# Kernel tuning notes

Measured on AMD Instinct MI355X. Metric: run time of the kernel, lower is better.

The kernel has to match this reference:

```python
import jax, jax.numpy as jnp
import numpy as np

BSIZE = 20
KEEP = 0.5  # 1 - dropout_rate


def setup_inputs() -> dict:
    key = jax.random.key(0)
    ks = jax.random.split(key, 8)
    B, N, C = 1, 262144, 128
    H = 300
    x = jax.random.normal(ks[0], (B, N, 2 * C), dtype=jnp.float32)
    ind = jax.random.randint(ks[1], (131072,), 0, B * N, dtype=jnp.int64)
    W1 = jax.random.normal(ks[2], (H, 2 * C), dtype=jnp.float32) * 0.05
    b1 = jnp.zeros((H,), dtype=jnp.float32)
    W2 = jax.random.normal(ks[3], (H, H), dtype=jnp.float32) * 0.05
    b2 = jnp.zeros((H,), dtype=jnp.float32)
    W3 = jax.random.normal(ks[4], (1, H), dtype=jnp.float32) * 0.05
    b3 = jnp.zeros((1,), dtype=jnp.float32)
    return {"x": x, "ind": ind, "W1": W1, "b1": b1, "W2": W2, "b2": b2, "W3": W3, "b3": b3}


def reference(x, ind, W1, b1, W2, b2, W3, b3):
    B, N, D = x.shape
    C = D // 2
    xf = x.reshape(B * N, D)
    xi = xf[ind]                     # [n, 2C] gathered joint samples
    n = ind.shape[0]

    def mlp(h, dkey):
        h = jax.nn.relu(h @ W1.T + b1)          # fc1 + relu
        h = h @ W2.T + b2                        # fc2
        mask = jax.random.bernoulli(dkey, KEEP, h.shape)
        h = jnp.where(mask, h / KEEP, jnp.float32(0))  # dropout
        h = jax.nn.relu(h)
        return h @ W3.T + b3                     # fc3 -> [n, 1]

    def step(acc, key):
        kp, k1, k2 = jax.random.split(key, 3)
        perm = jax.random.permutation(kp, n)
        z1 = mlp(xi, k1)
        # marginal: first-half features from ind, second-half from permuted ind
        xm = jnp.concatenate([xi[:, :C], xi[perm, C:]], axis=1)
        z2 = mlp(xm, k2)
        # mean(z1) - log(mean(exp(z2))) computed stably
        mi = jnp.mean(z1) - (jax.nn.logsumexp(z2) - jnp.log(jnp.float32(n)))
        return acc + mi, None

    keys = jax.random.split(jax.random.key(42), BSIZE)
    total, _ = jax.lax.scan(step, jnp.float32(0.0), keys)
    return total / BSIZE
```

## Files before the change

kernel.cpp:

```cpp
#include <hip/hip_runtime.h>
#include <hip/hip_fp16.h>


#define N_SAMP  131072
#define NMASK   (N_SAMP - 1)
#define HH      300
#define HPAD    320
#define DD      256
#define KPASS   20
#define PSTRIDE 320

#define OFF_S    ((size_t)0)
#define OFF_B1P  ((size_t)1024)
#define OFF_B2P  ((size_t)2304)
#define OFF_W3P  ((size_t)3584)
#define OFF_C2   ((size_t)4864)
#define OFF_W1B  ((size_t)8192)
#define OFF_W2B  (OFF_W1B + (size_t)163840)
#define OFF_P    (OFF_W2B + (size_t)204800)
#define OFF_Q    (OFF_P + (size_t)N_SAMP*PSTRIDE*2)

typedef _Float16 f16x8 __attribute__((ext_vector_type(8)));
typedef float    fx4   __attribute__((ext_vector_type(4)));

__global__ void prep_kernel(const float* __restrict__ W1, const float* __restrict__ b1,
                            const float* __restrict__ W2, const float* __restrict__ b2,
                            const float* __restrict__ W3, char* __restrict__ ws)
{
    double* S     = (double*)(ws + OFF_S);
    float* b1p    = (float*)(ws + OFF_B1P);
    float* b2p    = (float*)(ws + OFF_B2P);
    float* w3p    = (float*)(ws + OFF_W3P);
    float* c2p    = (float*)(ws + OFF_C2);
    _Float16* w1b = (_Float16*)(ws + OFF_W1B);
    _Float16* w2b = (_Float16*)(ws + OFF_W2B);
    int tid = blockIdx.x * blockDim.x + threadIdx.x;
    int nth = gridDim.x * blockDim.x;
    if (tid <= KPASS) S[tid] = 0.0;
    for (int i = tid; i < HPAD; i += nth) {
        b1p[i] = (i < HH) ? b1[i] : 0.f;
        b2p[i] = (i < HH) ? b2[i] : 0.f;
        w3p[i] = (i < HH) ? W3[i] : 0.f;
        c2p[i] = (i < HH) ? 2.8853900817779268f * W3[i] : 0.f;
    }
    for (int i = tid; i < 20 * 8 * 64 * 8; i += nth) {
        const int j = i & 7, lane = (i >> 3) & 63, rem = i >> 9;
        const int kt = rem & 7, nt = rem >> 3;
        const int n = nt * 16 + (lane & 15);
        const int k = kt * 32 + (lane >> 4) * 8 + j;
        w1b[i] = (n < HH) ? (_Float16)W1[n * DD + k] : (_Float16)0.f;
    }
    for (int i = tid; i < 4 * 50 * 64 * 8; i += nth) {
        const int j = i & 7, lane = (i >> 3) & 63, rem = i >> 9;
        const int nq = rem / 50, r2 = rem - nq * 50;
        const int kt = r2 / 5,  nn = r2 - kt * 5;
        const int nt = nq * 5 + nn;
        const int n = nt * 16 + (lane & 15);
        const int k = kt * 32 + (lane >> 4) * 8 + j;
        float v = 0.f;
        if (n < HH) {
            if (k < HH)       v = W2[n * HH + k];
            else if (k == HH) v = b2[n];
        }
        w2b[i] = (_Float16)v;
    }
}

__global__ __launch_bounds__(256, 2)
void fc1_kernel(const float* __restrict__ x, const int* __restrict__ ind,
                char* __restrict__ ws)
{
    const _Float16* w1b = (const _Float16*)(ws + OFF_W1B);
    const float* b1p    = (const float*)(ws + OFF_B1P);
    const int i0 = blockIdx.x * 128;

    __shared__ __align__(16) char lds[65536];
    _Float16* At  = (_Float16*)lds;
    _Float16* buf = (_Float16*)lds;

    const int t    = threadIdx.x;
    const int lane = t & 63, w = t >> 6;
    const int tx   = lane & 15, quad = lane >> 4;
    const int colw = w * 80;

    {
        const int m = t >> 1, c = t & 1;
        const int mt = m >> 4, ml = m & 15;
        const int r = ind[i0 + m];
        const float* xr = x + (size_t)r * DD;
        #pragma unroll
        for (int i = 0; i < 16; ++i) {
            const int ch = 2 * i + c;
            const int kt = ch >> 2, qd = ch & 3;
            const float4 f0 = *(const float4*)(xr + ch * 8);
            const float4 f1 = *(const float4*)(xr + ch * 8 + 4);
            f16x8 h;
            h[0] = (_Float16)f0.x; h[1] = (_Float16)f0.y;
            h[2] = (_Float16)f0.z; h[3] = (_Float16)f0.w;
            h[4] = (_Float16)f1.x; h[5] = (_Float16)f1.y;
            h[6] = (_Float16)f1.z; h[7] = (_Float16)f1.w;
            *(f16x8*)(At + ((size_t)(kt * 8 + mt) * 64 + ml * 4 + qd) * 8) = h;
        }
    }
    __syncthreads();

    #pragma unroll
    for (int ph = 0; ph < 2; ++ph) {
        fx4 acc[8][5] = {};
        #pragma unroll
        for (int kt = 0; kt < 4; ++kt) {
            const int ktg = ph * 4 + kt;
            f16x8 bf[5];
            #pragma unroll
            for (int n = 0; n < 5; ++n)
                bf[n] = *(const f16x8*)(w1b + ((size_t)((w * 5 + n) * 8 + ktg) * 64 + lane) * 8);
            #pragma unroll
            for (int mh = 0; mh < 2; ++mh) {
                f16x8 af[4];
                #pragma unroll
                for (int mi = 0; mi < 4; ++mi)
                    af[mi] = *(const f16x8*)(At + ((size_t)(ktg * 8 + mh * 4 + mi) * 64 + tx * 4 + quad) * 8);
                #pragma unroll
                for (int mi = 0; mi < 4; ++mi)
                    #pragma unroll
                    for (int n = 0; n < 5; ++n)
                        acc[mh * 4 + mi][n] =
                            __builtin_amdgcn_mfma_f32_16x16x32_f16(af[mi], bf[n], acc[mh * 4 + mi][n], 0, 0, 0);
            }
        }
        _Float16* out = (_Float16*)(ws + (ph ? OFF_Q : OFF_P));
        #pragma unroll
        for (int g = 0; g < 4; ++g) {
            __syncthreads();
            #pragma unroll
            for (int mi = 0; mi < 2; ++mi) {
                const int mt = g * 2 + mi;
                #pragma unroll
                for (int n = 0; n < 5; ++n) {
                    const int col = colw + n * 16 + tx;
                    const float bb = (ph == 0) ? b1p[col] : 0.f;
                    #pragma unroll
                    for (int r = 0; r < 4; ++r) {
                        const int row32 = mi * 16 + quad * 4 + r;
                        buf[row32 * 328 + col] = (_Float16)(acc[mt][n][r] + bb);
                    }
                }
            }
            __syncthreads();
            #pragma unroll
            for (int s5 = 0; s5 < 5; ++s5) {
                const int idx = t + s5 * 256;
                const int rr = idx / 40, cc = idx - rr * 40;
                *(uint4*)(out + (size_t)(i0 + g * 32 + rr) * PSTRIDE + cc * 8) =
                    *(const uint4*)(buf + rr * 328 + cc * 8);
            }
        }
        __syncthreads();
    }
}

__global__ __launch_bounds__(256, 3)
void fc23_kernel(char* __restrict__ ws)
{
    const _Float16* w2b = (const _Float16*)(ws + OFF_W2B);
    const float* w3p = (const float*)(ws + OFF_W3P);
    const float* c2p = (const float*)(ws + OFF_C2);
    const _Float16* P = (const _Float16*)(ws + OFF_P);
    const _Float16* Q = (const _Float16*)(ws + OFF_Q);
    double* S = (double*)(ws + OFF_S);

    const int p  = blockIdx.y;
    const int i0 = blockIdx.x * 64;
    const unsigned shift = (p == 0) ? 0u : (((unsigned)p * 2654435761u) & NMASK);

    __shared__ __align__(16) char lds[40960 + 1024];
    _Float16* At = (_Float16*)lds;
    float* part = (float*)(lds + 40960);

    const int t    = threadIdx.x;
    const int lane = t & 63, w = t >> 6;
    const int tx   = lane & 15, quad = lane >> 4;
    const int colw = w * 80;

    const _Float16* wb = w2b + (size_t)(w * 50) * 512 + (size_t)lane * 8;
    f16x8 bA[5], bB[5];
    #pragma unroll
    for (int n = 0; n < 5; ++n) bA[n] = *(const f16x8*)(wb + (size_t)n * 512);

    {
        const int c = t & 3, m = t >> 2;
        const int mt = m >> 4, ml = m & 15;
        const int prow = i0 + m;
        int ws_ = ml * 4 + c;  ws_ ^= (ws_ >> 3) & 3;
        const _Float16* pr = P + (size_t)prow * PSTRIDE;
        const _Float16* qr = Q + (size_t)(((unsigned)prow + shift) & NMASK) * PSTRIDE;
        #pragma unroll
        for (int i = 0; i < 10; ++i) {
            const int ch = c + 4 * i;
            f16x8 hp = *(const f16x8*)(pr + ch * 8);
            f16x8 hq = *(const f16x8*)(qr + ch * 8);
            f16x8 sv = hp + hq;
            sv = __builtin_elementwise_max(sv, (f16x8)(_Float16)0);
            if (i == 9 && c == 1) sv[4] = (_Float16)1.f;
            *(f16x8*)(At + ((size_t)(mt * 10 + i) * 64 + ws_) * 8) = sv;
        }
    }
    __syncthreads();

    int rs = tx * 4 + quad;  rs ^= (rs >> 3) & 3;

    fx4 acc[4][5] = {};
    #pragma unroll
    for (int kt = 0; kt < 10; ++kt) {
        f16x8* bc = (kt & 1) ? bB : bA;
        f16x8* bn = (kt & 1) ? bA : bB;
        if (kt < 9) {
            #pragma unroll
            for (int n = 0; n < 5; ++n)
                bn[n] = *(const f16x8*)(wb + (size_t)((kt + 1) * 5 + n) * 512);
        }
        f16x8 af[4];
        #pragma unroll
        for (int mi = 0; mi < 4; ++mi)
            af[mi] = *(const f16x8*)(At + ((size_t)(mi * 10 + kt) * 64 + rs) * 8);
        #pragma unroll
        for (int mi = 0; mi < 4; ++mi)
            #pragma unroll
            for (int n = 0; n < 5; ++n)
                acc[mi][n] =
                    __builtin_amdgcn_mfma_f32_16x16x32_f16(af[mi], bc[n], acc[mi][n], 0, 0, 0);
    }

    float w3v[5], c2v[5];
    #pragma unroll
    for (int n = 0; n < 5; ++n) {
        w3v[n] = w3p[colw + n * 16 + tx];
        c2v[n] = c2p[colw + n * 16 + tx];
    }
    #pragma unroll
    for (int mi = 0; mi < 4; ++mi) {
        float ps[4];
        if (p == 0) {
            ps[0] = ps[1] = ps[2] = ps[3] = 0.f;
            #pragma unroll
            for (int n = 0; n < 5; ++n)
                #pragma unroll
                for (int r = 0; r < 4; ++r)
                    ps[r] = fmaf(w3v[n], fmaxf(acc[mi][n][r], 0.f), ps[r]);
        } else {
            float prd[4] = {1.f, 1.f, 1.f, 1.f};
            #pragma unroll
            for (int n = 0; n < 5; ++n)
                #pragma unroll
                for (int r = 0; r < 4; ++r) {
                    const float hr = fmaxf(acc[mi][n][r], 0.f);
                    const float u  = __builtin_amdgcn_exp2f(c2v[n] * hr);
                    prd[r] *= fmaf(0.5f, u, 0.5f);
                }
            #pragma unroll
            for (int r = 0; r < 4; ++r)
                ps[r] = __builtin_amdgcn_logf(prd[r]);
        }
        #pragma unroll
        for (int r = 0; r < 4; ++r) {
            float v = ps[r];
            v += __shfl_xor(v, 1); v += __shfl_xor(v, 2);
            v += __shfl_xor(v, 4); v += __shfl_xor(v, 8);
            ps[r] = v;
        }
        if (tx == 0) {
            #pragma unroll
            for (int r = 0; r < 4; ++r)
                part[(mi * 16 + quad * 4 + r) * 4 + w] = ps[r];
        }
    }
    __syncthreads();

    if (t < 64) {
        const float4 pv = *(const float4*)(part + t * 4);
        const float s = pv.x + pv.y + pv.z + pv.w;
        float tot = (p == 0) ? s : __builtin_amdgcn_exp2f(s);
        tot += __shfl_xor(tot, 1);  tot += __shfl_xor(tot, 2);
        tot += __shfl_xor(tot, 4);  tot += __shfl_xor(tot, 8);
        tot += __shfl_xor(tot, 16); tot += __shfl_xor(tot, 32);
        if (t == 0) atomicAdd(&S[p], (double)tot);
    }
}

__global__ void fin_kernel(char* __restrict__ ws, float* __restrict__ out)
{
    if (threadIdx.x == 0 && blockIdx.x == 0) {
        const double* S = (const double*)(ws + OFF_S);
        double m1 = S[0] / (double)N_SAMP;
        double a = 0.0;
        for (int p = 1; p <= KPASS; ++p) a += log(S[p] / (double)N_SAMP);
        out[0] = (float)(m1 - a / (double)KPASS);
    }
}

extern "C" void kernel_launch(void* const* d_in, const int* in_sizes, int n_in,
                              void* d_out, int out_size, void* d_ws, size_t ws_size,
                              hipStream_t stream)
{
    const float* x  = (const float*)d_in[0];
    const int* ind  = (const int*)d_in[1];
    const float* W1 = (const float*)d_in[2];
    const float* b1 = (const float*)d_in[3];
    const float* W2 = (const float*)d_in[4];
    const float* b2 = (const float*)d_in[5];
    const float* W3 = (const float*)d_in[6];
    char* ws = (char*)d_ws;

    hipLaunchKernelGGL(prep_kernel, dim3(512), dim3(256), 0, stream, W1, b1, W2, b2, W3, ws);
    hipLaunchKernelGGL(fc1_kernel, dim3(N_SAMP / 128), dim3(256), 0, stream, x, ind, ws);
    hipLaunchKernelGGL(fc23_kernel, dim3(N_SAMP / 64, KPASS + 1), dim3(256), 0, stream, ws);
    hipLaunchKernelGGL(fin_kernel, dim3(1), dim3(64), 0, stream, ws, (float*)d_out);
}
```

Baseline: 1.118 ms.

## Stage P/Q tiles into LDS via direct global-to-LDS loads, combine in MFMA loop

The fc23 kernel now copies raw P and Q rows straight into LDS with global_load_lds instead of loading them through registers, adding, applying ReLU and storing. The add and ReLU move into the MFMA k-loop, done on LDS reads of both tiles. The bias-1 column is produced by adding 0.5 in each of the P and Q producers instead of being patched in. LDS use doubles to 80KB and occupancy drops from 3 to 2 blocks per CU, with extra LDS reads and vector ops inside the inner loop.

```diff
diff --git a/kernel.cpp b/kernel.cpp
--- a/kernel.cpp
+++ b/kernel.cpp
@@ -22,6 +22,13 @@
 
 typedef _Float16 f16x8 __attribute__((ext_vector_type(8)));
 typedef float    fx4   __attribute__((ext_vector_type(4)));
+
+__device__ __forceinline__ void gload_lds16(const void* g, void* l)
+{
+    __builtin_amdgcn_global_load_lds(
+        (const __attribute__((address_space(1))) void*)g,
+        (__attribute__((address_space(3))) void*)l, 16, 0, 0);
+}
 
 __global__ void prep_kernel(const float* __restrict__ W1, const float* __restrict__ b1,
                             const float* __restrict__ W2, const float* __restrict__ b2,
@@ -38,7 +45,7 @@
     int nth = gridDim.x * blockDim.x;
     if (tid <= KPASS) S[tid] = 0.0;
     for (int i = tid; i < HPAD; i += nth) {
-        b1p[i] = (i < HH) ? b1[i] : 0.f;
+        b1p[i] = (i < HH) ? b1[i] : ((i == HH) ? 0.5f : 0.f);
         b2p[i] = (i < HH) ? b2[i] : 0.f;
         w3p[i] = (i < HH) ? W3[i] : 0.f;
         c2p[i] = (i < HH) ? 2.8853900817779268f * W3[i] : 0.f;
@@ -138,7 +145,8 @@
                 #pragma unroll
                 for (int n = 0; n < 5; ++n) {
                     const int col = colw + n * 16 + tx;
-                    const float bb = (ph == 0) ? b1p[col] : 0.f;
+                    const float bb = (ph == 0) ? b1p[col]
+                                               : ((col == HH) ? 0.5f : 0.f);
                     #pragma unroll
                     for (int r = 0; r < 4; ++r) {
                         const int row32 = mi * 16 + quad * 4 + r;
@@ -159,7 +167,7 @@
     }
 }
 
-__global__ __launch_bounds__(256, 3)
+__global__ __launch_bounds__(256, 2)
 void fc23_kernel(char* __restrict__ ws)
 {
     const _Float16* w2b = (const _Float16*)(ws + OFF_W2B);
@@ -173,38 +181,37 @@
     const int i0 = blockIdx.x * 64;
     const unsigned shift = (p == 0) ? 0u : (((unsigned)p * 2654435761u) & NMASK);
 
-    __shared__ __align__(16) char lds[40960 + 1024];
-    _Float16* At = (_Float16*)lds;
-    float* part = (float*)(lds + 40960);
+    __shared__ __align__(16) char lds[81920];
+    _Float16* Pt = (_Float16*)lds;
+    _Float16* Qt = (_Float16*)(lds + 40960);
+    float* part  = (float*)lds;
 
     const int t    = threadIdx.x;
     const int lane = t & 63, w = t >> 6;
     const int tx   = lane & 15, quad = lane >> 4;
     const int colw = w * 80;
 
+    {
+        const int g = lane ^ ((lane >> 3) & 3);
+        const int prow = i0 + w * 16 + (g >> 2);
+        const unsigned qrow = ((unsigned)prow + shift) & NMASK;
+        const char* psrc = (const char*)(P + (size_t)prow * PSTRIDE) + (g & 3) * 16;
+        const char* qsrc = (const char*)(Q + (size_t)qrow * PSTRIDE) + (g & 3) * 16;
+        char* pdst = (char*)Pt + w * 10240;
+        char* qdst = (char*)Qt + w * 10240;
+        #pragma unroll
+        for (int kt = 0; kt < 10; ++kt) {
+            gload_lds16(psrc + kt * 64, pdst + kt * 1024);
+            gload_lds16(qsrc + kt * 64, qdst + kt * 1024);
+        }
+    }
+
     const _Float16* wb = w2b + (size_t)(w * 50) * 512 + (size_t)lane * 8;
     f16x8 bA[5], bB[5];
     #pragma unroll
     for (int n = 0; n < 5; ++n) bA[n] = *(const f16x8*)(wb + (size_t)n * 512);
 
-    {
-        const int c = t & 3, m = t >> 2;
-        const int mt = m >> 4, ml = m & 15;
-        const int prow = i0 + m;
-        int ws_ = ml * 4 + c;  ws_ ^= (ws_ >> 3) & 3;
-        const _Float16* pr = P + (size_t)prow * PSTRIDE;
-        const _Float16* qr = Q + (size_t)(((unsigned)prow + shift) & NMASK) * PSTRIDE;
-        #pragma unroll
-        for (int i = 0; i < 10; ++i) {
-            const int ch = c + 4 * i;
-            f16x8 hp = *(const f16x8*)(pr + ch * 8);
-            f16x8 hq = *(const f16x8*)(qr + ch * 8);
-            f16x8 sv = hp + hq;
-            sv = __builtin_elementwise_max(sv, (f16x8)(_Float16)0);
-            if (i == 9 && c == 1) sv[4] = (_Float16)1.f;
-            *(f16x8*)(At + ((size_t)(mt * 10 + i) * 64 + ws_) * 8) = sv;
-        }
-    }
+    asm volatile("s_waitcnt vmcnt(0)" ::: "memory");
     __syncthreads();
 
     int rs = tx * 4 + quad;  rs ^= (rs >> 3) & 3;
@@ -221,8 +228,13 @@
         }
         f16x8 af[4];
         #pragma unroll
-        for (int mi = 0; mi < 4; ++mi)
-            af[mi] = *(const f16x8*)(At + ((size_t)(mi * 10 + kt) * 64 + rs) * 8);
+        for (int mi = 0; mi < 4; ++mi) {
+            const size_t o = ((size_t)(mi * 10 + kt) * 64 + rs) * 8;
+            f16x8 ap = *(const f16x8*)(Pt + o);
+            f16x8 aq = *(const f16x8*)(Qt + o);
+            f16x8 sv = ap + aq;
+            af[mi] = __builtin_elementwise_max(sv, (f16x8)(_Float16)0);
+        }
         #pragma unroll
         for (int mi = 0; mi < 4; ++mi)
             #pragma unroll
@@ -237,6 +249,7 @@
         w3v[n] = w3p[colw + n * 16 + tx];
         c2v[n] = c2p[colw + n * 16 + tx];
     }
+    float psv[4][4];
     #pragma unroll
     for (int mi = 0; mi < 4; ++mi) {
         float ps[4];
@@ -266,13 +279,17 @@
             float v = ps[r];
             v += __shfl_xor(v, 1); v += __shfl_xor(v, 2);
             v += __shfl_xor(v, 4); v += __shfl_xor(v, 8);
-            ps[r] = v;
-        }
-        if (tx == 0) {
+            psv[mi][r] = v;
+        }
+    }
+    __syncthreads();
+
+    if (tx == 0) {
+        #pragma unroll
+        for (int mi = 0; mi < 4; ++mi)
             #pragma unroll
             for (int r = 0; r < 4; ++r)
-                part[(mi * 16 + quad * 4 + r) * 4 + w] = ps[r];
-        }
+                part[(mi * 16 + quad * 4 + r) * 4 + w] = psv[mi][r];
     }
     __syncthreads();
 
```

After: 1.279 ms. 14.4% more time.
